# Performance work log

Hardware: AMD Instinct MI355X
Metric: run time of the kernel (lower is better)

The kernel has to match this reference:

```python
import jax, jax.numpy as jnp
import numpy as np

T, B, H, D = 128, 8, 8, 64


def setup_inputs() -> dict:
    key = jax.random.key(0)
    kA, kB, kS = jax.random.split(key, 3)
    # Gated-delta transition matrices: near-identity contractions so the
    # length-T matrix-product recurrence is numerically stable, mimicking
    # A_t = gamma_t * (I - beta_t k_t k_t^T) of the gated delta rule.
    eye = jnp.eye(D, dtype=jnp.float32)
    A = 0.9 * eye + 0.06 * jax.random.normal(kA, (T, B, H, D, D), dtype=jnp.float32)
    Bm = jax.random.normal(kB, (T, B, H, D, D), dtype=jnp.float32)
    init_state = jax.random.normal(kS, (B, H, D, D), dtype=jnp.float32)
    return {"A": A, "Bm": Bm, "init_state": init_state}


def reference(A, Bm, init_state):
    """Gated delta rule recurrence S_t = S_{t-1} @ A_t + B_t for all t,
    computed with a parallel associative scan (Blelloch-equivalent).

    A:  [T,B,H,D,D] transition matrices
    Bm: [T,B,H,D,D] additive updates
    init_state: [B,H,D,D]
    returns states: [T,B,H,D,D]
    """
    def combine(e1, e2):
        # apply e1 first, then e2:
        # (S A1 + B1) A2 + B2 = S (A1 A2) + (B1 A2 + B2)
        A1, B1 = e1
        A2, B2 = e2
        A12 = jnp.einsum('tbhij,tbhjk->tbhik', A1, A2)
        B12 = jnp.einsum('tbhij,tbhjk->tbhik', B1, A2) + B2
        return (A12, B12)

    cumA, cumB = jax.lax.associative_scan(combine, (A, Bm), axis=0)
    # S_t = init_state @ cumA_t + cumB_t
    states = jnp.einsum('bhij,tbhjk->tbhik', init_state, cumA) + cumB
    return states
```

## Files before the change

kernel.cpp:

```cpp
#include <hip/hip_runtime.h>


constexpr int kT = 128;
constexpr int kBH = 64;
constexpr int kD = 64;
constexpr int kTile = kD * kD;
constexpr int kNC = 16;
constexpr int kCH = 8;

typedef __attribute__((ext_vector_type(8))) short short8;
typedef __attribute__((ext_vector_type(4))) float f32x4;
using u32 = unsigned int;

union U8 { u32 u[4]; short8 s; };

__device__ __forceinline__ f32x4 mfma16(short8 a, short8 b, f32x4 c) {
  return __builtin_amdgcn_mfma_f32_16x16x32_bf16(a, b, c, 0, 0, 0);
}

__device__ __forceinline__ void pk_split(float a, float b, u32& h, u32& l) {
  u32 hu;
  asm("v_cvt_pk_bf16_f32 %0, %1, %2" : "=v"(hu) : "v"(a), "v"(b));
  const float ra = a - __uint_as_float(hu << 16);
  const float rb = b - __uint_as_float(hu & 0xffff0000u);
  u32 lu;
  asm("v_cvt_pk_bf16_f32 %0, %1, %2" : "=v"(lu) : "v"(ra), "v"(rb));
  h = hu;
  l = lu;
}

__device__ __forceinline__ short8 gather_frag(u32 p01, u32 p23, u32 q01, u32 q23,
                                              int ad0, int ad1, bool lowh) {
  U8 r;
  int x, y;
  x = __builtin_amdgcn_ds_bpermute(ad0, (int)p01);
  y = __builtin_amdgcn_ds_bpermute(ad0, (int)q01);
  r.u[0] = (u32)(lowh ? x : y);
  x = __builtin_amdgcn_ds_bpermute(ad0, (int)p23);
  y = __builtin_amdgcn_ds_bpermute(ad0, (int)q23);
  r.u[1] = (u32)(lowh ? x : y);
  x = __builtin_amdgcn_ds_bpermute(ad1, (int)p01);
  y = __builtin_amdgcn_ds_bpermute(ad1, (int)q01);
  r.u[2] = (u32)(lowh ? x : y);
  x = __builtin_amdgcn_ds_bpermute(ad1, (int)p23);
  y = __builtin_amdgcn_ds_bpermute(ad1, (int)q23);
  r.u[3] = (u32)(lowh ? x : y);
  return r.s;
}

__device__ __forceinline__ void read_afragT(const float* sAbuf, int row, int k0,
                                            short8& ah, short8& al) {
  const float* base = sAbuf + k0 * 64 + row;
  float d0 = base[0], d1 = base[64], d2 = base[128], d3 = base[192];
  float d4 = base[256], d5 = base[320], d6 = base[384], d7 = base[448];
  U8 h, l;
  u32 hu, lu;
  pk_split(d0, d1, hu, lu); h.u[0] = hu; l.u[0] = lu;
  pk_split(d2, d3, hu, lu); h.u[1] = hu; l.u[1] = lu;
  pk_split(d4, d5, hu, lu); h.u[2] = hu; l.u[2] = lu;
  pk_split(d6, d7, hu, lu); h.u[3] = hu; l.u[3] = lu;
  ah = h.s; al = l.s;
}

#define ISSUE_A(PTRA, SBUF)                                                     \
  do {                                                                          \
    const float* gp_ = (PTRA);                                                  \
    _Pragma("unroll") for (int it_ = 0; it_ < 4; ++it_) {                       \
      const int off_ = (w * 4 + it_) * 256;                                     \
      __builtin_amdgcn_global_load_lds(                                         \
          (const __attribute__((address_space(1))) u32*)(gp_ + off_ + lane * 4),\
          (__attribute__((address_space(3))) u32*)&(SBUF)[off_],                \
          16, 0, 0);                                                            \
    }                                                                           \
  } while (0)

#define LOAD_B4(PTRB)                                                          \
  do {                                                                         \
    const float* Bt_ = (PTRB);                                                 \
    b0 = *reinterpret_cast<const f32x4*>(Bt_ + rowbase + 0 * 16 + q * 4);      \
    b1 = *reinterpret_cast<const f32x4*>(Bt_ + rowbase + 1 * 16 + q * 4);      \
    b2 = *reinterpret_cast<const f32x4*>(Bt_ + rowbase + 2 * 16 + q * 4);      \
    b3 = *reinterpret_cast<const f32x4*>(Bt_ + rowbase + 3 * 16 + q * 4);      \
  } while (0)

#define FOLD_STEP(J, SCUR, SNXT)                                              \
  do {                                                                        \
    const int j_ = (J);                                                       \
    const bool more_ = (j_ + 1 < nS);                                         \
    f32x4 npa[4], npb[4];                                                     \
    npb[0] = b0; npb[1] = b1; npb[2] = b2; npb[3] = b3;                       \
    _Pragma("unroll") for (int cm = 0; cm < 4; ++cm)                          \
        npa[cm] = (f32x4){0.f, 0.f, 0.f, 0.f};                                \
    if (more_) {                                                              \
      ISSUE_A(srcA + (size_t)(e0 + (long)(j_ + 2) * elemStride) * kTile, SNXT); \
      LOAD_B4(srcB + (size_t)(e0 + (long)(j_ + 2) * elemStride) * kTile);     \
      __builtin_amdgcn_sched_barrier(0);                                      \
    }                                                                         \
    _Pragma("unroll") for (int ks = 0; ks < 2; ++ks) {                        \
      u32 pa01h, pa01l, pa23h, pa23l, qa01h, qa01l, qa23h, qa23l;             \
      u32 pb01h, pb01l, pb23h, pb23l, qb01h, qb01l, qb23h, qb23l;             \
      pk_split(apa[2 * ks][0], apa[2 * ks][1], pa01h, pa01l);                 \
      pk_split(apa[2 * ks][2], apa[2 * ks][3], pa23h, pa23l);                 \
      pk_split(apa[2 * ks + 1][0], apa[2 * ks + 1][1], qa01h, qa01l);         \
      pk_split(apa[2 * ks + 1][2], apa[2 * ks + 1][3], qa23h, qa23l);         \
      pk_split(apb[2 * ks][0], apb[2 * ks][1], pb01h, pb01l);                 \
      pk_split(apb[2 * ks][2], apb[2 * ks][3], pb23h, pb23l);                 \
      pk_split(apb[2 * ks + 1][0], apb[2 * ks + 1][1], qb01h, qb01l);         \
      pk_split(apb[2 * ks + 1][2], apb[2 * ks + 1][3], qb23h, qb23l);         \
      const short8 bah = gather_frag(pa01h, pa23h, qa01h, qa23h, ad0, ad1, lowh); \
      const short8 bal = gather_frag(pa01l, pa23l, qa01l, qa23l, ad0, ad1, lowh); \
      const short8 bbh = gather_frag(pb01h, pb23h, qb01h, qb23h, ad0, ad1, lowh); \
      const short8 bbl = gather_frag(pb01l, pb23l, qb01l, qb23l, ad0, ad1, lowh); \
      _Pragma("unroll") for (int cm = 0; cm < 4; ++cm) {                      \
        short8 ah, al;                                                        \
        read_afragT(&(SCUR)[0], cm * 16 + l15, ks * 32 + q * 8, ah, al);      \
        npa[cm] = mfma16(ah, bah, npa[cm]);                                   \
        npa[cm] = mfma16(ah, bal, npa[cm]);                                   \
        npa[cm] = mfma16(al, bah, npa[cm]);                                   \
        npb[cm] = mfma16(ah, bbh, npb[cm]);                                   \
        npb[cm] = mfma16(ah, bbl, npb[cm]);                                   \
        npb[cm] = mfma16(al, bbh, npb[cm]);                                   \
      }                                                                       \
    }                                                                         \
    _Pragma("unroll") for (int cm = 0; cm < 4; ++cm) {                        \
      apa[cm] = npa[cm];                                                      \
      apb[cm] = npb[cm];                                                      \
    }                                                                         \
    if (more_) __syncthreads();                                               \
  } while (0)

__global__ __attribute__((amdgpu_flat_work_group_size(256, 256),
                          amdgpu_waves_per_eu(4, 4)))
void gdr_fold(const float* __restrict__ srcA, const float* __restrict__ srcB,
              float* __restrict__ dstA, float* __restrict__ dstB,
              int perChain, long chainBase, long idxBase, long elemStride,
              int nElem) {
  __shared__ float sA0[4096], sA1[4096];

  const int tid = threadIdx.x;
  const int lane = tid & 63, w = tid >> 6;
  const int q = lane >> 4, l15 = lane & 15;
  const int bh = blockIdx.x / perChain, id = blockIdx.x % perChain;
  const long e0 = (long)bh * chainBase + (long)id * idxBase;
  const int rowbase = (w * 16 + l15) * 64;
  const int ad0 = (l15 + ((lane >> 4) & 1) * 32) * 4;
  const int ad1 = ad0 + 64;
  const bool lowh = lane < 32;
  const int nS = nElem - 1;

  f32x4 apa[4], apb[4];
  {
    const float* At = srcA + (size_t)e0 * kTile;
    const float* Bt = srcB + (size_t)e0 * kTile;
#pragma unroll
    for (int cm = 0; cm < 4; ++cm) {
      apa[cm] = *reinterpret_cast<const f32x4*>(At + rowbase + cm * 16 + q * 4);
      apb[cm] = *reinterpret_cast<const f32x4*>(Bt + rowbase + cm * 16 + q * 4);
    }
  }

  f32x4 b0, b1, b2, b3;
  ISSUE_A(srcA + (size_t)(e0 + elemStride) * kTile, sA0);
  LOAD_B4(srcB + (size_t)(e0 + elemStride) * kTile);
  __syncthreads();

  int j = 0;
  while (true) {
    FOLD_STEP(j, sA0, sA1);
    if (++j >= nS) break;
    FOLD_STEP(j, sA1, sA0);
    if (++j >= nS) break;
  }

  float* pao = dstA + (size_t)blockIdx.x * kTile;
  float* pbo = dstB + (size_t)blockIdx.x * kTile;
#pragma unroll
  for (int cm = 0; cm < 4; ++cm) {
    *reinterpret_cast<f32x4*>(pao + rowbase + cm * 16 + q * 4) = apa[cm];
    *reinterpret_cast<f32x4*>(pbo + rowbase + cm * 16 + q * 4) = apb[cm];
  }
}

#define SCAN_STEP(I, SCUR, SNXT)                                              \
  do {                                                                        \
    const int i_ = (I);                                                       \
    const bool more_ = (i_ + 1 < nSteps);                                     \
    f32x4 nacc[4];                                                            \
    nacc[0] = b0; nacc[1] = b1; nacc[2] = b2; nacc[3] = b3;                   \
    if (more_) {                                                              \
      ISSUE_A(srcA + (size_t)(e0 + (long)(i_ + 1) * elemStride) * kTile, SNXT); \
      LOAD_B4(srcB + (size_t)(e0 + (long)(i_ + 1) * elemStride) * kTile);     \
      __builtin_amdgcn_sched_barrier(0);                                      \
    }                                                                         \
    _Pragma("unroll") for (int ks = 0; ks < 2; ++ks) {                        \
      u32 p01h, p01l, p23h, p23l, q01h, q01l, q23h, q23l;                     \
      pk_split(acc[2 * ks][0], acc[2 * ks][1], p01h, p01l);                   \
      pk_split(acc[2 * ks][2], acc[2 * ks][3], p23h, p23l);                   \
      pk_split(acc[2 * ks + 1][0], acc[2 * ks + 1][1], q01h, q01l);           \
      pk_split(acc[2 * ks + 1][2], acc[2 * ks + 1][3], q23h, q23l);           \
      const short8 bfh = gather_frag(p01h, p23h, q01h, q23h, ad0, ad1, lowh); \
      const short8 bfl = gather_frag(p01l, p23l, q01l, q23l, ad0, ad1, lowh); \
      _Pragma("unroll") for (int cm = 0; cm < 4; ++cm) {                      \
        short8 ah, al;                                                        \
        read_afragT(&(SCUR)[0], cm * 16 + l15, ks * 32 + q * 8, ah, al);      \
        nacc[cm] = mfma16(ah, bfh, nacc[cm]);                                 \
        nacc[cm] = mfma16(ah, bfl, nacc[cm]);                                 \
        nacc[cm] = mfma16(al, bfh, nacc[cm]);                                 \
      }                                                                       \
    }                                                                         \
    const int t_ = tBase + (i_ + 1) * tStep - 1;                              \
    float* o_ = out + ((size_t)t_ * kBH + bh) * kTile;                        \
    _Pragma("unroll") for (int cm = 0; cm < 4; ++cm) {                        \
      *reinterpret_cast<f32x4*>(o_ + rowbase + cm * 16 + q * 4) = nacc[cm];   \
      acc[cm] = nacc[cm];                                                     \
    }                                                                         \
    if (more_) __syncthreads();                                               \
  } while (0)

__global__ __attribute__((amdgpu_flat_work_group_size(256, 256),
                          amdgpu_waves_per_eu(4, 4)))
void gdr_scan(const float* __restrict__ srcA, const float* __restrict__ srcB,
              const float* __restrict__ S0, float* __restrict__ out,
              int perChain, long chainBase, long idxBase, long elemStride,
              int nSteps, int tbMul, int tStep) {
  __shared__ float sA0[4096], sA1[4096];

  const int tid = threadIdx.x;
  const int lane = tid & 63, w = tid >> 6;
  const int q = lane >> 4, l15 = lane & 15;
  const int bh = blockIdx.x / perChain, id = blockIdx.x % perChain;
  const long e0 = (long)bh * chainBase + (long)id * idxBase;
  const int tBase = id * tbMul;
  const int rowbase = (w * 16 + l15) * 64;
  const int ad0 = (l15 + ((lane >> 4) & 1) * 32) * 4;
  const int ad1 = ad0 + 64;
  const bool lowh = lane < 32;

  f32x4 acc[4];
  {
    const float* Sb = (tBase == 0) ? (S0 + (size_t)bh * kTile)
                                   : (out + ((size_t)(tBase - 1) * kBH + bh) * kTile);
#pragma unroll
    for (int cm = 0; cm < 4; ++cm)
      acc[cm] = *reinterpret_cast<const f32x4*>(Sb + rowbase + cm * 16 + q * 4);
  }

  f32x4 b0, b1, b2, b3;
  ISSUE_A(srcA + (size_t)e0 * kTile, sA0);
  LOAD_B4(srcB + (size_t)e0 * kTile);
  __syncthreads();

  int i = 0;
  while (true) {
    SCAN_STEP(i, sA0, sA1);
    if (++i >= nSteps) break;
    SCAN_STEP(i, sA1, sA0);
    if (++i >= nSteps) break;
  }
}

extern "C" void kernel_launch(void* const* d_in, const int* in_sizes, int n_in,
                              void* d_out, int out_size, void* d_ws, size_t ws_size,
                              hipStream_t stream) {
  const float* A  = (const float*)d_in[0];
  const float* Bm = (const float*)d_in[1];
  const float* S0 = (const float*)d_in[2];
  float* out = (float*)d_out;

  float* PA = (float*)d_ws;
  float* PB = PA + (size_t)kBH * kNC * kTile;

  gdr_fold<<<dim3(kBH * kNC), dim3(256), 0, stream>>>(
      A, Bm, PA, PB, kNC, 1L, (long)kCH * kBH, (long)kBH, kCH);
  gdr_scan<<<dim3(kBH), dim3(256), 0, stream>>>(
      PA, PB, S0, out, 1, (long)kNC, 0L, 1L, kNC, 0, kCH);
  gdr_scan<<<dim3(kBH * kNC), dim3(256), 0, stream>>>(
      A, Bm, S0, out, kNC, 1L, (long)kCH * kBH, (long)kBH, kCH - 1, kCH, 1);
}
```

Before: 161.2 us.

## Triple-buffer A tiles in LDS with partial vmcnt waits instead of full syncs

Moves the fold and scan kernels from double- to triple-buffered LDS for the A tiles, prefetching two steps ahead. B tiles are ping-ponged between two register sets. The full __syncthreads after each step becomes an explicit s_waitcnt vmcnt(N) plus s_barrier, so later loads can stay in flight. The aim is to hide global-load latency on the serial recurrence chain. In exchange it uses more LDS and registers (waves_per_eu relaxed to 3), and correctness depends on the hand-counted vmcnt values.

```diff
diff --git a/kernel.cpp b/kernel.cpp
--- a/kernel.cpp
+++ b/kernel.cpp
@@ -65,37 +65,55 @@
 #define ISSUE_A(PTRA, SBUF)                                                     \
   do {                                                                          \
     const float* gp_ = (PTRA);                                                  \
+    float* sb_ = (SBUF);                                                        \
     _Pragma("unroll") for (int it_ = 0; it_ < 4; ++it_) {                       \
       const int off_ = (w * 4 + it_) * 256;                                     \
       __builtin_amdgcn_global_load_lds(                                         \
           (const __attribute__((address_space(1))) u32*)(gp_ + off_ + lane * 4),\
-          (__attribute__((address_space(3))) u32*)&(SBUF)[off_],                \
+          (__attribute__((address_space(3))) u32*)(sb_ + off_),                 \
           16, 0, 0);                                                            \
     }                                                                           \
   } while (0)
 
-#define LOAD_B4(PTRB)                                                          \
+#define LOAD_B4_INTO(R0, R1, R2, R3, PTRB)                                     \
   do {                                                                         \
     const float* Bt_ = (PTRB);                                                 \
-    b0 = *reinterpret_cast<const f32x4*>(Bt_ + rowbase + 0 * 16 + q * 4);      \
-    b1 = *reinterpret_cast<const f32x4*>(Bt_ + rowbase + 1 * 16 + q * 4);      \
-    b2 = *reinterpret_cast<const f32x4*>(Bt_ + rowbase + 2 * 16 + q * 4);      \
-    b3 = *reinterpret_cast<const f32x4*>(Bt_ + rowbase + 3 * 16 + q * 4);      \
-  } while (0)
-
-#define FOLD_STEP(J, SCUR, SNXT)                                              \
+    R0 = *reinterpret_cast<const f32x4*>(Bt_ + rowbase + 0 * 16 + q * 4);      \
+    R1 = *reinterpret_cast<const f32x4*>(Bt_ + rowbase + 1 * 16 + q * 4);      \
+    R2 = *reinterpret_cast<const f32x4*>(Bt_ + rowbase + 2 * 16 + q * 4);      \
+    R3 = *reinterpret_cast<const f32x4*>(Bt_ + rowbase + 3 * 16 + q * 4);      \
+  } while (0)
+
+#define SB0() __builtin_amdgcn_sched_barrier(0)
+
+#define VM_WAIT_BARRIER(NSTR)                                   \
+  do {                                                          \
+    SB0();                                                      \
+    asm volatile("s_waitcnt vmcnt(" NSTR ")" ::: "memory");     \
+    SB0();                                                      \
+    __builtin_amdgcn_s_barrier();                               \
+    SB0();                                                      \
+  } while (0)
+
+#define FOLD_STEP(J, C0, C1, C2, C3, I0, I1, I2, I3)                          \
   do {                                                                        \
     const int j_ = (J);                                                       \
     const bool more_ = (j_ + 1 < nS);                                         \
+    if (more_) {                                                              \
+      const int eB_ = (j_ + 2 <= eMax) ? j_ + 2 : eMax;                       \
+      const int eA_ = (j_ + 3 <= eMax) ? j_ + 3 : eMax;                       \
+      LOAD_B4_INTO(I0, I1, I2, I3,                                            \
+                   srcB + (size_t)(e0 + (long)eB_ * elemStride) * kTile);     \
+      SB0();                                                                  \
+      ISSUE_A(srcA + (size_t)(e0 + (long)eA_ * elemStride) * kTile,           \
+              &sA[cTgt][0]);                                                  \
+      SB0();                                                                  \
+    }                                                                         \
     f32x4 npa[4], npb[4];                                                     \
-    npb[0] = b0; npb[1] = b1; npb[2] = b2; npb[3] = b3;                       \
+    npb[0] = C0; npb[1] = C1; npb[2] = C2; npb[3] = C3;                       \
     _Pragma("unroll") for (int cm = 0; cm < 4; ++cm)                          \
         npa[cm] = (f32x4){0.f, 0.f, 0.f, 0.f};                                \
-    if (more_) {                                                              \
-      ISSUE_A(srcA + (size_t)(e0 + (long)(j_ + 2) * elemStride) * kTile, SNXT); \
-      LOAD_B4(srcB + (size_t)(e0 + (long)(j_ + 2) * elemStride) * kTile);     \
-      __builtin_amdgcn_sched_barrier(0);                                      \
-    }                                                                         \
+    const float* sCur_ = &sA[cCur][0];                                        \
     _Pragma("unroll") for (int ks = 0; ks < 2; ++ks) {                        \
       u32 pa01h, pa01l, pa23h, pa23l, qa01h, qa01l, qa23h, qa23l;             \
       u32 pb01h, pb01l, pb23h, pb23l, qb01h, qb01l, qb23h, qb23l;             \
@@ -113,7 +131,7 @@
       const short8 bbl = gather_frag(pb01l, pb23l, qb01l, qb23l, ad0, ad1, lowh); \
       _Pragma("unroll") for (int cm = 0; cm < 4; ++cm) {                      \
         short8 ah, al;                                                        \
-        read_afragT(&(SCUR)[0], cm * 16 + l15, ks * 32 + q * 8, ah, al);      \
+        read_afragT(sCur_, cm * 16 + l15, ks * 32 + q * 8, ah, al);           \
         npa[cm] = mfma16(ah, bah, npa[cm]);                                   \
         npa[cm] = mfma16(ah, bal, npa[cm]);                                   \
         npa[cm] = mfma16(al, bah, npa[cm]);                                   \
@@ -126,16 +144,18 @@
       apa[cm] = npa[cm];                                                      \
       apb[cm] = npb[cm];                                                      \
     }                                                                         \
-    if (more_) __syncthreads();                                               \
+    if (more_) VM_WAIT_BARRIER("8");                                          \
+    cCur = (cCur == 2) ? 0 : cCur + 1;                                        \
+    cTgt = (cTgt == 2) ? 0 : cTgt + 1;                                        \
   } while (0)
 
 __global__ __attribute__((amdgpu_flat_work_group_size(256, 256),
-                          amdgpu_waves_per_eu(4, 4)))
+                          amdgpu_waves_per_eu(3, 4)))
 void gdr_fold(const float* __restrict__ srcA, const float* __restrict__ srcB,
               float* __restrict__ dstA, float* __restrict__ dstB,
               int perChain, long chainBase, long idxBase, long elemStride,
               int nElem) {
-  __shared__ float sA0[4096], sA1[4096];
+  __shared__ float sA[3][4096];
 
   const int tid = threadIdx.x;
   const int lane = tid & 63, w = tid >> 6;
@@ -147,6 +167,7 @@
   const int ad1 = ad0 + 64;
   const bool lowh = lane < 32;
   const int nS = nElem - 1;
+  const int eMax = nElem - 1;
 
   f32x4 apa[4], apb[4];
   {
@@ -159,16 +180,28 @@
     }
   }
 
-  f32x4 b0, b1, b2, b3;
-  ISSUE_A(srcA + (size_t)(e0 + elemStride) * kTile, sA0);
-  LOAD_B4(srcB + (size_t)(e0 + elemStride) * kTile);
-  __syncthreads();
-
+  f32x4 r0a, r0b, r0c, r0d;
+  f32x4 r1a, r1b, r1c, r1d;
+
+  {
+    const int e2 = (2 <= eMax) ? 2 : eMax;
+    LOAD_B4_INTO(r1a, r1b, r1c, r1d, srcB + (size_t)(e0 + elemStride) * kTile);
+    SB0();
+    ISSUE_A(srcA + (size_t)(e0 + elemStride) * kTile, &sA[1][0]);
+    ISSUE_A(srcA + (size_t)(e0 + (long)e2 * elemStride) * kTile, &sA[2][0]);
+    SB0();
+    asm volatile("s_waitcnt vmcnt(4)" ::: "memory");
+    SB0();
+    __builtin_amdgcn_s_barrier();
+    SB0();
+  }
+
+  int cCur = 1, cTgt = 0;
   int j = 0;
   while (true) {
-    FOLD_STEP(j, sA0, sA1);
+    FOLD_STEP(j, r1a, r1b, r1c, r1d, r0a, r0b, r0c, r0d);
     if (++j >= nS) break;
-    FOLD_STEP(j, sA1, sA0);
+    FOLD_STEP(j, r0a, r0b, r0c, r0d, r1a, r1b, r1c, r1d);
     if (++j >= nS) break;
   }
 
@@ -181,17 +214,23 @@
   }
 }
 
-#define SCAN_STEP(I, SCUR, SNXT)                                              \
+#define SCAN_STEP(I, C0, C1, C2, C3, I0, I1, I2, I3)                          \
   do {                                                                        \
     const int i_ = (I);                                                       \
     const bool more_ = (i_ + 1 < nSteps);                                     \
+    if (more_) {                                                              \
+      const int eB_ = (i_ + 1 <= eMax) ? i_ + 1 : eMax;                       \
+      const int eA_ = (i_ + 2 <= eMax) ? i_ + 2 : eMax;                       \
+      LOAD_B4_INTO(I0, I1, I2, I3,                                            \
+                   srcB + (size_t)(e0 + (long)eB_ * elemStride) * kTile);     \
+      SB0();                                                                  \
+      ISSUE_A(srcA + (size_t)(e0 + (long)eA_ * elemStride) * kTile,           \
+              &sA[cTgt][0]);                                                  \
+      SB0();                                                                  \
+    }                                                                         \
     f32x4 nacc[4];                                                            \
-    nacc[0] = b0; nacc[1] = b1; nacc[2] = b2; nacc[3] = b3;                   \
-    if (more_) {                                                              \
-      ISSUE_A(srcA + (size_t)(e0 + (long)(i_ + 1) * elemStride) * kTile, SNXT); \
-      LOAD_B4(srcB + (size_t)(e0 + (long)(i_ + 1) * elemStride) * kTile);     \
-      __builtin_amdgcn_sched_barrier(0);                                      \
-    }                                                                         \
+    nacc[0] = C0; nacc[1] = C1; nacc[2] = C2; nacc[3] = C3;                   \
+    const float* sCur_ = &sA[cCur][0];                                        \
     _Pragma("unroll") for (int ks = 0; ks < 2; ++ks) {                        \
       u32 p01h, p01l, p23h, p23l, q01h, q01l, q23h, q23l;                     \
       pk_split(acc[2 * ks][0], acc[2 * ks][1], p01h, p01l);                   \
@@ -202,7 +241,7 @@
       const short8 bfl = gather_frag(p01l, p23l, q01l, q23l, ad0, ad1, lowh); \
       _Pragma("unroll") for (int cm = 0; cm < 4; ++cm) {                      \
         short8 ah, al;                                                        \
-        read_afragT(&(SCUR)[0], cm * 16 + l15, ks * 32 + q * 8, ah, al);      \
+        read_afragT(sCur_, cm * 16 + l15, ks * 32 + q * 8, ah, al);           \
         nacc[cm] = mfma16(ah, bfh, nacc[cm]);                                 \
         nacc[cm] = mfma16(ah, bfl, nacc[cm]);                                 \
         nacc[cm] = mfma16(al, bfh, nacc[cm]);                                 \
@@ -214,16 +253,18 @@
       *reinterpret_cast<f32x4*>(o_ + rowbase + cm * 16 + q * 4) = nacc[cm];   \
       acc[cm] = nacc[cm];                                                     \
     }                                                                         \
-    if (more_) __syncthreads();                                               \
+    if (more_) VM_WAIT_BARRIER("12");                                         \
+    cCur = (cCur == 2) ? 0 : cCur + 1;                                        \
+    cTgt = (cTgt == 2) ? 0 : cTgt + 1;                                        \
   } while (0)
 
 __global__ __attribute__((amdgpu_flat_work_group_size(256, 256),
-                          amdgpu_waves_per_eu(4, 4)))
+                          amdgpu_waves_per_eu(3, 4)))
 void gdr_scan(const float* __restrict__ srcA, const float* __restrict__ srcB,
               const float* __restrict__ S0, float* __restrict__ out,
               int perChain, long chainBase, long idxBase, long elemStride,
               int nSteps, int tbMul, int tStep) {
-  __shared__ float sA0[4096], sA1[4096];
+  __shared__ float sA[3][4096];
 
   const int tid = threadIdx.x;
   const int lane = tid & 63, w = tid >> 6;
@@ -235,6 +276,7 @@
   const int ad0 = (l15 + ((lane >> 4) & 1) * 32) * 4;
   const int ad1 = ad0 + 64;
   const bool lowh = lane < 32;
+  const int eMax = nSteps - 1;
 
   f32x4 acc[4];
   {
@@ -245,16 +287,28 @@
       acc[cm] = *reinterpret_cast<const f32x4*>(Sb + rowbase + cm * 16 + q * 4);
   }
 
-  f32x4 b0, b1, b2, b3;
-  ISSUE_A(srcA + (size_t)e0 * kTile, sA0);
-  LOAD_B4(srcB + (size_t)e0 * kTile);
-  __syncthreads();
-
+  f32x4 r0a, r0b, r0c, r0d;
+  f32x4 r1a, r1b, r1c, r1d;
+
+  {
+    const int e1 = (1 <= eMax) ? 1 : eMax;
+    LOAD_B4_INTO(r0a, r0b, r0c, r0d, srcB + (size_t)e0 * kTile);
+    SB0();
+    ISSUE_A(srcA + (size_t)e0 * kTile, &sA[0][0]);
+    ISSUE_A(srcA + (size_t)(e0 + (long)e1 * elemStride) * kTile, &sA[1][0]);
+    SB0();
+    asm volatile("s_waitcnt vmcnt(4)" ::: "memory");
+    SB0();
+    __builtin_amdgcn_s_barrier();
+    SB0();
+  }
+
+  int cCur = 0, cTgt = 2;
   int i = 0;
   while (true) {
-    SCAN_STEP(i, sA0, sA1);
+    SCAN_STEP(i, r0a, r0b, r0c, r0d, r1a, r1b, r1c, r1d);
     if (++i >= nSteps) break;
-    SCAN_STEP(i, sA1, sA0);
+    SCAN_STEP(i, r1a, r1b, r1c, r1d, r0a, r0b, r0c, r0d);
     if (++i >= nSteps) break;
   }
 }
```

Measured after the change: 172.8 us. +7.2%, slower.

## Halve chunk length, prefetch whole chunk to padded LDS, specialize kernels

Applied to the files above, without the earlier changes.

Changes the three-phase chunked scan from 16 chunks of 8 to 32 chunks of 4. The fold and scan kernels now prefetch all three A tiles of a chunk at once into LDS with a 65-float row pitch, meant to avoid bank conflicts on the transposed fragment reads. They then run fully unrolled with a single barrier instead of a double-buffered loop. The middle sequential scan gets longer (32 steps) but the parallel phases get shorter. LDS use rises, and the 4-byte global_load_lds calls add many more load instructions.

```diff
diff --git a/kernel.cpp b/kernel.cpp
--- a/kernel.cpp
+++ b/kernel.cpp
@@ -5,8 +5,9 @@
 constexpr int kBH = 64;
 constexpr int kD = 64;
 constexpr int kTile = kD * kD;
-constexpr int kNC = 16;
-constexpr int kCH = 8;
+constexpr int kNC = 32;
+constexpr int kCH = 4;
+constexpr int kP = 65;
 
 typedef __attribute__((ext_vector_type(8))) short short8;
 typedef __attribute__((ext_vector_type(4))) float f32x4;
@@ -17,6 +18,8 @@
 __device__ __forceinline__ f32x4 mfma16(short8 a, short8 b, f32x4 c) {
   return __builtin_amdgcn_mfma_f32_16x16x32_bf16(a, b, c, 0, 0, 0);
 }
+
+#define SB0() __builtin_amdgcn_sched_barrier(0)
 
 __device__ __forceinline__ void pk_split(float a, float b, u32& h, u32& l) {
   u32 hu;
@@ -48,11 +51,11 @@
   return r.s;
 }
 
-__device__ __forceinline__ void read_afragT(const float* sAbuf, int row, int k0,
-                                            short8& ah, short8& al) {
-  const float* base = sAbuf + k0 * 64 + row;
-  float d0 = base[0], d1 = base[64], d2 = base[128], d3 = base[192];
-  float d4 = base[256], d5 = base[320], d6 = base[384], d7 = base[448];
+__device__ __forceinline__ void read_afragT65(const float* sAbuf, int row, int k0,
+                                              short8& ah, short8& al) {
+  const float* base = sAbuf + k0 * kP + row;
+  float d0 = base[0 * kP], d1 = base[1 * kP], d2 = base[2 * kP], d3 = base[3 * kP];
+  float d4 = base[4 * kP], d5 = base[5 * kP], d6 = base[6 * kP], d7 = base[7 * kP];
   U8 h, l;
   u32 hu, lu;
   pk_split(d0, d1, hu, lu); h.u[0] = hu; l.u[0] = lu;
@@ -62,40 +65,35 @@
   ah = h.s; al = l.s;
 }
 
-#define ISSUE_A(PTRA, SBUF)                                                     \
+#define ISSUE_A65(PTRA, SBUF)                                                   \
   do {                                                                          \
     const float* gp_ = (PTRA);                                                  \
-    _Pragma("unroll") for (int it_ = 0; it_ < 4; ++it_) {                       \
-      const int off_ = (w * 4 + it_) * 256;                                     \
+    float* sb_ = (SBUF);                                                        \
+    _Pragma("unroll") for (int it_ = 0; it_ < 16; ++it_) {                      \
+      const int row_ = w * 16 + it_;                                            \
       __builtin_amdgcn_global_load_lds(                                         \
-          (const __attribute__((address_space(1))) u32*)(gp_ + off_ + lane * 4),\
-          (__attribute__((address_space(3))) u32*)&(SBUF)[off_],                \
-          16, 0, 0);                                                            \
+          (const __attribute__((address_space(1))) u32*)(gp_ + row_ * 64 + lane), \
+          (__attribute__((address_space(3))) u32*)(sb_ + row_ * kP),            \
+          4, 0, 0);                                                             \
     }                                                                           \
   } while (0)
 
-#define LOAD_B4(PTRB)                                                          \
+#define LOAD_B4_INTO(R0, R1, R2, R3, PTRB)                                     \
   do {                                                                         \
     const float* Bt_ = (PTRB);                                                 \
-    b0 = *reinterpret_cast<const f32x4*>(Bt_ + rowbase + 0 * 16 + q * 4);      \
-    b1 = *reinterpret_cast<const f32x4*>(Bt_ + rowbase + 1 * 16 + q * 4);      \
-    b2 = *reinterpret_cast<const f32x4*>(Bt_ + rowbase + 2 * 16 + q * 4);      \
-    b3 = *reinterpret_cast<const f32x4*>(Bt_ + rowbase + 3 * 16 + q * 4);      \
-  } while (0)
-
-#define FOLD_STEP(J, SCUR, SNXT)                                              \
+    R0 = *reinterpret_cast<const f32x4*>(Bt_ + rowbase + 0 * 16 + q * 4);      \
+    R1 = *reinterpret_cast<const f32x4*>(Bt_ + rowbase + 1 * 16 + q * 4);      \
+    R2 = *reinterpret_cast<const f32x4*>(Bt_ + rowbase + 2 * 16 + q * 4);      \
+    R3 = *reinterpret_cast<const f32x4*>(Bt_ + rowbase + 3 * 16 + q * 4);      \
+  } while (0)
+
+#define STEP_FOLD(SA, C0, C1, C2, C3)                                         \
   do {                                                                        \
-    const int j_ = (J);                                                       \
-    const bool more_ = (j_ + 1 < nS);                                         \
     f32x4 npa[4], npb[4];                                                     \
-    npb[0] = b0; npb[1] = b1; npb[2] = b2; npb[3] = b3;                       \
+    npb[0] = C0; npb[1] = C1; npb[2] = C2; npb[3] = C3;                       \
     _Pragma("unroll") for (int cm = 0; cm < 4; ++cm)                          \
         npa[cm] = (f32x4){0.f, 0.f, 0.f, 0.f};                                \
-    if (more_) {                                                              \
-      ISSUE_A(srcA + (size_t)(e0 + (long)(j_ + 2) * elemStride) * kTile, SNXT); \
-      LOAD_B4(srcB + (size_t)(e0 + (long)(j_ + 2) * elemStride) * kTile);     \
-      __builtin_amdgcn_sched_barrier(0);                                      \
-    }                                                                         \
+    const float* sCur_ = &(SA)[0];                                            \
     _Pragma("unroll") for (int ks = 0; ks < 2; ++ks) {                        \
       u32 pa01h, pa01l, pa23h, pa23l, qa01h, qa01l, qa23h, qa23l;             \
       u32 pb01h, pb01l, pb23h, pb23l, qb01h, qb01l, qb23h, qb23l;             \
@@ -113,7 +111,7 @@
       const short8 bbl = gather_frag(pb01l, pb23l, qb01l, qb23l, ad0, ad1, lowh); \
       _Pragma("unroll") for (int cm = 0; cm < 4; ++cm) {                      \
         short8 ah, al;                                                        \
-        read_afragT(&(SCUR)[0], cm * 16 + l15, ks * 32 + q * 8, ah, al);      \
+        read_afragT65(sCur_, cm * 16 + l15, ks * 32 + q * 8, ah, al);         \
         npa[cm] = mfma16(ah, bah, npa[cm]);                                   \
         npa[cm] = mfma16(ah, bal, npa[cm]);                                   \
         npa[cm] = mfma16(al, bah, npa[cm]);                                   \
@@ -126,27 +124,23 @@
       apa[cm] = npa[cm];                                                      \
       apb[cm] = npb[cm];                                                      \
     }                                                                         \
-    if (more_) __syncthreads();                                               \
   } while (0)
 
 __global__ __attribute__((amdgpu_flat_work_group_size(256, 256),
-                          amdgpu_waves_per_eu(4, 4)))
-void gdr_fold(const float* __restrict__ srcA, const float* __restrict__ srcB,
-              float* __restrict__ dstA, float* __restrict__ dstB,
-              int perChain, long chainBase, long idxBase, long elemStride,
-              int nElem) {
-  __shared__ float sA0[4096], sA1[4096];
+                          amdgpu_waves_per_eu(3, 4)))
+void gdr_fold4(const float* __restrict__ srcA, const float* __restrict__ srcB,
+               float* __restrict__ dstA, float* __restrict__ dstB) {
+  __shared__ float sA1[64 * kP], sA2[64 * kP], sA3[64 * kP];
 
   const int tid = threadIdx.x;
   const int lane = tid & 63, w = tid >> 6;
   const int q = lane >> 4, l15 = lane & 15;
-  const int bh = blockIdx.x / perChain, id = blockIdx.x % perChain;
-  const long e0 = (long)bh * chainBase + (long)id * idxBase;
+  const int bh = blockIdx.x / kNC, ck = blockIdx.x % kNC;
+  const long e0 = (long)bh + (long)ck * (kCH * kBH);
   const int rowbase = (w * 16 + l15) * 64;
   const int ad0 = (l15 + ((lane >> 4) & 1) * 32) * 4;
   const int ad1 = ad0 + 64;
   const bool lowh = lane < 32;
-  const int nS = nElem - 1;
 
   f32x4 apa[4], apb[4];
   {
@@ -158,19 +152,26 @@
       apb[cm] = *reinterpret_cast<const f32x4*>(Bt + rowbase + cm * 16 + q * 4);
     }
   }
-
-  f32x4 b0, b1, b2, b3;
-  ISSUE_A(srcA + (size_t)(e0 + elemStride) * kTile, sA0);
-  LOAD_B4(srcB + (size_t)(e0 + elemStride) * kTile);
-  __syncthreads();
-
-  int j = 0;
-  while (true) {
-    FOLD_STEP(j, sA0, sA1);
-    if (++j >= nS) break;
-    FOLD_STEP(j, sA1, sA0);
-    if (++j >= nS) break;
-  }
+  SB0();
+  ISSUE_A65(srcA + (size_t)(e0 + 1 * kBH) * kTile, sA1);
+  ISSUE_A65(srcA + (size_t)(e0 + 2 * kBH) * kTile, sA2);
+  ISSUE_A65(srcA + (size_t)(e0 + 3 * kBH) * kTile, sA3);
+  SB0();
+  f32x4 r1a, r1b, r1c, r1d, r2a, r2b, r2c, r2d, r3a, r3b, r3c, r3d;
+  LOAD_B4_INTO(r1a, r1b, r1c, r1d, srcB + (size_t)(e0 + 1 * kBH) * kTile);
+  SB0();
+  LOAD_B4_INTO(r2a, r2b, r2c, r2d, srcB + (size_t)(e0 + 2 * kBH) * kTile);
+  SB0();
+  LOAD_B4_INTO(r3a, r3b, r3c, r3d, srcB + (size_t)(e0 + 3 * kBH) * kTile);
+  SB0();
+  asm volatile("s_waitcnt vmcnt(12)" ::: "memory");
+  SB0();
+  __builtin_amdgcn_s_barrier();
+  SB0();
+
+  STEP_FOLD(sA1, r1a, r1b, r1c, r1d);
+  STEP_FOLD(sA2, r2a, r2b, r2c, r2d);
+  STEP_FOLD(sA3, r3a, r3b, r3c, r3d);
 
   float* pao = dstA + (size_t)blockIdx.x * kTile;
   float* pbo = dstB + (size_t)blockIdx.x * kTile;
@@ -181,17 +182,11 @@
   }
 }
 
-#define SCAN_STEP(I, SCUR, SNXT)                                              \
+#define STEP_SCAN(SA, C0, C1, C2, C3, TI)                                     \
   do {                                                                        \
-    const int i_ = (I);                                                       \
-    const bool more_ = (i_ + 1 < nSteps);                                     \
     f32x4 nacc[4];                                                            \
-    nacc[0] = b0; nacc[1] = b1; nacc[2] = b2; nacc[3] = b3;                   \
-    if (more_) {                                                              \
-      ISSUE_A(srcA + (size_t)(e0 + (long)(i_ + 1) * elemStride) * kTile, SNXT); \
-      LOAD_B4(srcB + (size_t)(e0 + (long)(i_ + 1) * elemStride) * kTile);     \
-      __builtin_amdgcn_sched_barrier(0);                                      \
-    }                                                                         \
+    nacc[0] = C0; nacc[1] = C1; nacc[2] = C2; nacc[3] = C3;                   \
+    const float* sCur_ = &(SA)[0];                                            \
     _Pragma("unroll") for (int ks = 0; ks < 2; ++ks) {                        \
       u32 p01h, p01l, p23h, p23l, q01h, q01l, q23h, q23l;                     \
       pk_split(acc[2 * ks][0], acc[2 * ks][1], p01h, p01l);                   \
@@ -202,35 +197,32 @@
       const short8 bfl = gather_frag(p01l, p23l, q01l, q23l, ad0, ad1, lowh); \
       _Pragma("unroll") for (int cm = 0; cm < 4; ++cm) {                      \
         short8 ah, al;                                                        \
-        read_afragT(&(SCUR)[0], cm * 16 + l15, ks * 32 + q * 8, ah, al);      \
+        read_afragT65(sCur_, cm * 16 + l15, ks * 32 + q * 8, ah, al);         \
         nacc[cm] = mfma16(ah, bfh, nacc[cm]);                                 \
         nacc[cm] = mfma16(ah, bfl, nacc[cm]);                                 \
         nacc[cm] = mfma16(al, bfh, nacc[cm]);                                 \
       }                                                                       \
     }                                                                         \
-    const int t_ = tBase + (i_ + 1) * tStep - 1;                              \
+    const int t_ = tBase + (TI);                                              \
     float* o_ = out + ((size_t)t_ * kBH + bh) * kTile;                        \
     _Pragma("unroll") for (int cm = 0; cm < 4; ++cm) {                        \
       *reinterpret_cast<f32x4*>(o_ + rowbase + cm * 16 + q * 4) = nacc[cm];   \
       acc[cm] = nacc[cm];                                                     \
     }                                                                         \
-    if (more_) __syncthreads();                                               \
   } while (0)
 
 __global__ __attribute__((amdgpu_flat_work_group_size(256, 256),
-                          amdgpu_waves_per_eu(4, 4)))
-void gdr_scan(const float* __restrict__ srcA, const float* __restrict__ srcB,
-              const float* __restrict__ S0, float* __restrict__ out,
-              int perChain, long chainBase, long idxBase, long elemStride,
-              int nSteps, int tbMul, int tStep) {
-  __shared__ float sA0[4096], sA1[4096];
+                          amdgpu_waves_per_eu(3, 4)))
+void gdr_scan4(const float* __restrict__ srcA, const float* __restrict__ srcB,
+               const float* __restrict__ S0, float* __restrict__ out) {
+  __shared__ float sA1[64 * kP], sA2[64 * kP], sA3[64 * kP];
 
   const int tid = threadIdx.x;
   const int lane = tid & 63, w = tid >> 6;
   const int q = lane >> 4, l15 = lane & 15;
-  const int bh = blockIdx.x / perChain, id = blockIdx.x % perChain;
-  const long e0 = (long)bh * chainBase + (long)id * idxBase;
-  const int tBase = id * tbMul;
+  const int bh = blockIdx.x / kNC, ck = blockIdx.x % kNC;
+  const long e0 = (long)bh + (long)ck * (kCH * kBH);
+  const int tBase = ck * kCH;
   const int rowbase = (w * 16 + l15) * 64;
   const int ad0 = (l15 + ((lane >> 4) & 1) * 32) * 4;
   const int ad1 = ad0 + 64;
@@ -244,18 +236,125 @@
     for (int cm = 0; cm < 4; ++cm)
       acc[cm] = *reinterpret_cast<const f32x4*>(Sb + rowbase + cm * 16 + q * 4);
   }
+  SB0();
+  ISSUE_A65(srcA + (size_t)e0 * kTile, sA1);
+  ISSUE_A65(srcA + (size_t)(e0 + 1 * kBH) * kTile, sA2);
+  ISSUE_A65(srcA + (size_t)(e0 + 2 * kBH) * kTile, sA3);
+  SB0();
+  f32x4 r1a, r1b, r1c, r1d, r2a, r2b, r2c, r2d, r3a, r3b, r3c, r3d;
+  LOAD_B4_INTO(r1a, r1b, r1c, r1d, srcB + (size_t)e0 * kTile);
+  SB0();
+  LOAD_B4_INTO(r2a, r2b, r2c, r2d, srcB + (size_t)(e0 + 1 * kBH) * kTile);
+  SB0();
+  LOAD_B4_INTO(r3a, r3b, r3c, r3d, srcB + (size_t)(e0 + 2 * kBH) * kTile);
+  SB0();
+  asm volatile("s_waitcnt vmcnt(12)" ::: "memory");
+  SB0();
+  __builtin_amdgcn_s_barrier();
+  SB0();
+
+  STEP_SCAN(sA1, r1a, r1b, r1c, r1d, 0);
+  STEP_SCAN(sA2, r2a, r2b, r2c, r2d, 1);
+  STEP_SCAN(sA3, r3a, r3b, r3c, r3d, 2);
+}
+
+__device__ __forceinline__ void read_afragT64(const float* sAbuf, int row, int k0,
+                                              short8& ah, short8& al) {
+  const float* base = sAbuf + k0 * 64 + row;
+  float d0 = base[0], d1 = base[64], d2 = base[128], d3 = base[192];
+  float d4 = base[256], d5 = base[320], d6 = base[384], d7 = base[448];
+  U8 h, l;
+  u32 hu, lu;
+  pk_split(d0, d1, hu, lu); h.u[0] = hu; l.u[0] = lu;
+  pk_split(d2, d3, hu, lu); h.u[1] = hu; l.u[1] = lu;
+  pk_split(d4, d5, hu, lu); h.u[2] = hu; l.u[2] = lu;
+  pk_split(d6, d7, hu, lu); h.u[3] = hu; l.u[3] = lu;
+  ah = h.s; al = l.s;
+}
+
+#define ISSUE_A16(PTRA, SBUF)                                                   \
+  do {                                                                          \
+    const float* gp_ = (PTRA);                                                  \
+    float* sb_ = (SBUF);                                                        \
+    _Pragma("unroll") for (int it_ = 0; it_ < 4; ++it_) {                       \
+      const int off_ = (w * 4 + it_) * 256;                                     \
+      __builtin_amdgcn_global_load_lds(                                         \
+          (const __attribute__((address_space(1))) u32*)(gp_ + off_ + lane * 4),\
+          (__attribute__((address_space(3))) u32*)(sb_ + off_),                 \
+          16, 0, 0);                                                            \
+    }                                                                           \
+  } while (0)
+
+#define SEQ_STEP(I, SCUR, SNXT)                                               \
+  do {                                                                        \
+    const int i_ = (I);                                                       \
+    const bool more_ = (i_ + 1 < kNC);                                        \
+    f32x4 nacc[4];                                                            \
+    nacc[0] = b0; nacc[1] = b1; nacc[2] = b2; nacc[3] = b3;                   \
+    if (more_) {                                                              \
+      ISSUE_A16(srcA + (size_t)(e0 + i_ + 1) * kTile, SNXT);                  \
+      LOAD_B4_INTO(b0, b1, b2, b3, srcB + (size_t)(e0 + i_ + 1) * kTile);     \
+      SB0();                                                                  \
+    }                                                                         \
+    _Pragma("unroll") for (int ks = 0; ks < 2; ++ks) {                        \
+      u32 p01h, p01l, p23h, p23l, q01h, q01l, q23h, q23l;                     \
+      pk_split(acc[2 * ks][0], acc[2 * ks][1], p01h, p01l);                   \
+      pk_split(acc[2 * ks][2], acc[2 * ks][3], p23h, p23l);                   \
+      pk_split(acc[2 * ks + 1][0], acc[2 * ks + 1][1], q01h, q01l);           \
+      pk_split(acc[2 * ks + 1][2], acc[2 * ks + 1][3], q23h, q23l);           \
+      const short8 bfh = gather_frag(p01h, p23h, q01h, q23h, ad0, ad1, lowh); \
+      const short8 bfl = gather_frag(p01l, p23l, q01l, q23l, ad0, ad1, lowh); \
+      _Pragma("unroll") for (int cm = 0; cm < 4; ++cm) {                      \
+        short8 ah, al;                                                        \
+        read_afragT64(&(SCUR)[0], cm * 16 + l15, ks * 32 + q * 8, ah, al);    \
+        nacc[cm] = mfma16(ah, bfh, nacc[cm]);                                 \
+        nacc[cm] = mfma16(ah, bfl, nacc[cm]);                                 \
+        nacc[cm] = mfma16(al, bfh, nacc[cm]);                                 \
+      }                                                                       \
+    }                                                                         \
+    const int t_ = (i_ + 1) * kCH - 1;                                        \
+    float* o_ = out + ((size_t)t_ * kBH + bh) * kTile;                        \
+    _Pragma("unroll") for (int cm = 0; cm < 4; ++cm) {                        \
+      *reinterpret_cast<f32x4*>(o_ + rowbase + cm * 16 + q * 4) = nacc[cm];   \
+      acc[cm] = nacc[cm];                                                     \
+    }                                                                         \
+    if (more_) __syncthreads();                                               \
+  } while (0)
+
+__global__ __launch_bounds__(256, 4) void gdr_scan_seq(
+    const float* __restrict__ srcA, const float* __restrict__ srcB,
+    const float* __restrict__ S0, float* __restrict__ out) {
+  __shared__ float sA0[4096], sA1b[4096];
+
+  const int tid = threadIdx.x;
+  const int lane = tid & 63, w = tid >> 6;
+  const int q = lane >> 4, l15 = lane & 15;
+  const int bh = blockIdx.x;
+  const long e0 = (long)bh * kNC;
+  const int rowbase = (w * 16 + l15) * 64;
+  const int ad0 = (l15 + ((lane >> 4) & 1) * 32) * 4;
+  const int ad1 = ad0 + 64;
+  const bool lowh = lane < 32;
+
+  f32x4 acc[4];
+  {
+    const float* Sb = S0 + (size_t)bh * kTile;
+#pragma unroll
+    for (int cm = 0; cm < 4; ++cm)
+      acc[cm] = *reinterpret_cast<const f32x4*>(Sb + rowbase + cm * 16 + q * 4);
+  }
 
   f32x4 b0, b1, b2, b3;
-  ISSUE_A(srcA + (size_t)e0 * kTile, sA0);
-  LOAD_B4(srcB + (size_t)e0 * kTile);
+  ISSUE_A16(srcA + (size_t)e0 * kTile, sA0);
+  LOAD_B4_INTO(b0, b1, b2, b3, srcB + (size_t)e0 * kTile);
   __syncthreads();
 
   int i = 0;
   while (true) {
-    SCAN_STEP(i, sA0, sA1);
-    if (++i >= nSteps) break;
-    SCAN_STEP(i, sA1, sA0);
-    if (++i >= nSteps) break;
+    SEQ_STEP(i, sA0, sA1b);
+    if (++i >= kNC) break;
+    SEQ_STEP(i, sA1b, sA0);
+    if (++i >= kNC) break;
   }
 }
 
@@ -270,10 +369,7 @@
   float* PA = (float*)d_ws;
   float* PB = PA + (size_t)kBH * kNC * kTile;
 
-  gdr_fold<<<dim3(kBH * kNC), dim3(256), 0, stream>>>(
-      A, Bm, PA, PB, kNC, 1L, (long)kCH * kBH, (long)kBH, kCH);
-  gdr_scan<<<dim3(kBH), dim3(256), 0, stream>>>(
-      PA, PB, S0, out, 1, (long)kNC, 0L, 1L, kNC, 0, kCH);
-  gdr_scan<<<dim3(kBH * kNC), dim3(256), 0, stream>>>(
-      A, Bm, S0, out, kNC, 1L, (long)kCH * kBH, (long)kBH, kCH - 1, kCH, 1);
-}
+  gdr_fold4<<<dim3(kBH * kNC), dim3(256), 0, stream>>>(A, Bm, PA, PB);
+  gdr_scan_seq<<<dim3(kBH), dim3(256), 0, stream>>>(PA, PB, S0, out);
+  gdr_scan4<<<dim3(kBH * kNC), dim3(256), 0, stream>>>(A, Bm, S0, out);
+}
```

Result: slower. 197.7 us (+22.7%).

## Pad LDS A tiles to stride 65 and replace bpermute gathers with permlane swaps

Applied to the files above, without the earlier changes.

Pads the shared-memory copy of each A tile to a row stride of 65 floats so the transposed column reads in read_afragT spread across LDS banks instead of colliding. Because the padded rows are no longer 16-byte aligned, the global-to-LDS async load now issues sixteen 4-byte transfers per wave instead of four 16-byte ones. Separately, the accumulator-to-B-fragment gather switches from ds_bpermute through LDS to v_permlane32/16_swap register shuffles, which keeps those shuffles off the LDS path. The risks are the larger number of small load instructions and the assumption that the permlane shuffle reproduces the old gather layout exactly.

```diff
diff --git a/kernel.cpp b/kernel.cpp
--- a/kernel.cpp
+++ b/kernel.cpp
@@ -7,6 +7,7 @@
 constexpr int kTile = kD * kD;
 constexpr int kNC = 16;
 constexpr int kCH = 8;
+constexpr int kP = 65;
 
 typedef __attribute__((ext_vector_type(8))) short short8;
 typedef __attribute__((ext_vector_type(4))) float f32x4;
@@ -29,30 +30,34 @@
   l = lu;
 }
 
-__device__ __forceinline__ short8 gather_frag(u32 p01, u32 p23, u32 q01, u32 q23,
-                                              int ad0, int ad1, bool lowh) {
+__device__ __forceinline__ void rowpat(u32 v, u32& oa, u32& ob) {
+  u32 d = v, s = v;
+  asm("v_permlane32_swap_b32 %0, %1" : "+v"(d), "+v"(s));
+  asm("v_permlane16_swap_b32 %0, %1" : "+v"(d), "+v"(s));
+  oa = d;
+  ob = s;
+}
+
+__device__ __forceinline__ short8 gather_frag_pl(u32 p01, u32 p23, u32 q01, u32 q23,
+                                                 bool lowh) {
+  u32 x0a, x0b, x1a, x1b, y0a, y0b, y1a, y1b;
+  rowpat(p01, x0a, x0b);
+  rowpat(p23, x1a, x1b);
+  rowpat(q01, y0a, y0b);
+  rowpat(q23, y1a, y1b);
   U8 r;
-  int x, y;
-  x = __builtin_amdgcn_ds_bpermute(ad0, (int)p01);
-  y = __builtin_amdgcn_ds_bpermute(ad0, (int)q01);
-  r.u[0] = (u32)(lowh ? x : y);
-  x = __builtin_amdgcn_ds_bpermute(ad0, (int)p23);
-  y = __builtin_amdgcn_ds_bpermute(ad0, (int)q23);
-  r.u[1] = (u32)(lowh ? x : y);
-  x = __builtin_amdgcn_ds_bpermute(ad1, (int)p01);
-  y = __builtin_amdgcn_ds_bpermute(ad1, (int)q01);
-  r.u[2] = (u32)(lowh ? x : y);
-  x = __builtin_amdgcn_ds_bpermute(ad1, (int)p23);
-  y = __builtin_amdgcn_ds_bpermute(ad1, (int)q23);
-  r.u[3] = (u32)(lowh ? x : y);
+  r.u[0] = lowh ? x0a : y0a;
+  r.u[1] = lowh ? x1a : y1a;
+  r.u[2] = lowh ? x0b : y0b;
+  r.u[3] = lowh ? x1b : y1b;
   return r.s;
 }
 
-__device__ __forceinline__ void read_afragT(const float* sAbuf, int row, int k0,
-                                            short8& ah, short8& al) {
-  const float* base = sAbuf + k0 * 64 + row;
-  float d0 = base[0], d1 = base[64], d2 = base[128], d3 = base[192];
-  float d4 = base[256], d5 = base[320], d6 = base[384], d7 = base[448];
+__device__ __forceinline__ void read_afragT65(const float* sAbuf, int row, int k0,
+                                              short8& ah, short8& al) {
+  const float* base = sAbuf + k0 * kP + row;
+  float d0 = base[0 * kP], d1 = base[1 * kP], d2 = base[2 * kP], d3 = base[3 * kP];
+  float d4 = base[4 * kP], d5 = base[5 * kP], d6 = base[6 * kP], d7 = base[7 * kP];
   U8 h, l;
   u32 hu, lu;
   pk_split(d0, d1, hu, lu); h.u[0] = hu; l.u[0] = lu;
@@ -62,15 +67,16 @@
   ah = h.s; al = l.s;
 }
 
-#define ISSUE_A(PTRA, SBUF)                                                     \
+#define ISSUE_A65(PTRA, SBUF)                                                   \
   do {                                                                          \
     const float* gp_ = (PTRA);                                                  \
-    _Pragma("unroll") for (int it_ = 0; it_ < 4; ++it_) {                       \
-      const int off_ = (w * 4 + it_) * 256;                                     \
+    float* sb_ = (SBUF);                                                        \
+    _Pragma("unroll") for (int it_ = 0; it_ < 16; ++it_) {                      \
+      const int row_ = w * 16 + it_;                                            \
       __builtin_amdgcn_global_load_lds(                                         \
-          (const __attribute__((address_space(1))) u32*)(gp_ + off_ + lane * 4),\
-          (__attribute__((address_space(3))) u32*)&(SBUF)[off_],                \
-          16, 0, 0);                                                            \
+          (const __attribute__((address_space(1))) u32*)(gp_ + row_ * 64 + lane), \
+          (__attribute__((address_space(3))) u32*)(sb_ + row_ * kP),            \
+          4, 0, 0);                                                             \
     }                                                                           \
   } while (0)
 
@@ -92,7 +98,7 @@
     _Pragma("unroll") for (int cm = 0; cm < 4; ++cm)                          \
         npa[cm] = (f32x4){0.f, 0.f, 0.f, 0.f};                                \
     if (more_) {                                                              \
-      ISSUE_A(srcA + (size_t)(e0 + (long)(j_ + 2) * elemStride) * kTile, SNXT); \
+      ISSUE_A65(srcA + (size_t)(e0 + (long)(j_ + 2) * elemStride) * kTile, SNXT); \
       LOAD_B4(srcB + (size_t)(e0 + (long)(j_ + 2) * elemStride) * kTile);     \
       __builtin_amdgcn_sched_barrier(0);                                      \
     }                                                                         \
@@ -107,13 +113,13 @@
       pk_split(apb[2 * ks][2], apb[2 * ks][3], pb23h, pb23l);                 \
       pk_split(apb[2 * ks + 1][0], apb[2 * ks + 1][1], qb01h, qb01l);         \
       pk_split(apb[2 * ks + 1][2], apb[2 * ks + 1][3], qb23h, qb23l);         \
-      const short8 bah = gather_frag(pa01h, pa23h, qa01h, qa23h, ad0, ad1, lowh); \
-      const short8 bal = gather_frag(pa01l, pa23l, qa01l, qa23l, ad0, ad1, lowh); \
-      const short8 bbh = gather_frag(pb01h, pb23h, qb01h, qb23h, ad0, ad1, lowh); \
-      const short8 bbl = gather_frag(pb01l, pb23l, qb01l, qb23l, ad0, ad1, lowh); \
+      const short8 bah = gather_frag_pl(pa01h, pa23h, qa01h, qa23h, lowh);    \
+      const short8 bal = gather_frag_pl(pa01l, pa23l, qa01l, qa23l, lowh);    \
+      const short8 bbh = gather_frag_pl(pb01h, pb23h, qb01h, qb23h, lowh);    \
+      const short8 bbl = gather_frag_pl(pb01l, pb23l, qb01l, qb23l, lowh);    \
       _Pragma("unroll") for (int cm = 0; cm < 4; ++cm) {                      \
         short8 ah, al;                                                        \
-        read_afragT(&(SCUR)[0], cm * 16 + l15, ks * 32 + q * 8, ah, al);      \
+        read_afragT65(&(SCUR)[0], cm * 16 + l15, ks * 32 + q * 8, ah, al);    \
         npa[cm] = mfma16(ah, bah, npa[cm]);                                   \
         npa[cm] = mfma16(ah, bal, npa[cm]);                                   \
         npa[cm] = mfma16(al, bah, npa[cm]);                                   \
@@ -129,13 +135,11 @@
     if (more_) __syncthreads();                                               \
   } while (0)
 
-__global__ __attribute__((amdgpu_flat_work_group_size(256, 256),
-                          amdgpu_waves_per_eu(4, 4)))
-void gdr_fold(const float* __restrict__ srcA, const float* __restrict__ srcB,
-              float* __restrict__ dstA, float* __restrict__ dstB,
-              int perChain, long chainBase, long idxBase, long elemStride,
-              int nElem) {
-  __shared__ float sA0[4096], sA1[4096];
+__global__ __launch_bounds__(256, 4) void gdr_fold(
+    const float* __restrict__ srcA, const float* __restrict__ srcB,
+    float* __restrict__ dstA, float* __restrict__ dstB,
+    int perChain, long chainBase, long idxBase, long elemStride, int nElem) {
+  __shared__ float sA0[64 * kP], sA1[64 * kP];
 
   const int tid = threadIdx.x;
   const int lane = tid & 63, w = tid >> 6;
@@ -143,8 +147,6 @@
   const int bh = blockIdx.x / perChain, id = blockIdx.x % perChain;
   const long e0 = (long)bh * chainBase + (long)id * idxBase;
   const int rowbase = (w * 16 + l15) * 64;
-  const int ad0 = (l15 + ((lane >> 4) & 1) * 32) * 4;
-  const int ad1 = ad0 + 64;
   const bool lowh = lane < 32;
   const int nS = nElem - 1;
 
@@ -160,7 +162,7 @@
   }
 
   f32x4 b0, b1, b2, b3;
-  ISSUE_A(srcA + (size_t)(e0 + elemStride) * kTile, sA0);
+  ISSUE_A65(srcA + (size_t)(e0 + elemStride) * kTile, sA0);
   LOAD_B4(srcB + (size_t)(e0 + elemStride) * kTile);
   __syncthreads();
 
@@ -188,7 +190,7 @@
     f32x4 nacc[4];                                                            \
     nacc[0] = b0; nacc[1] = b1; nacc[2] = b2; nacc[3] = b3;                   \
     if (more_) {                                                              \
-      ISSUE_A(srcA + (size_t)(e0 + (long)(i_ + 1) * elemStride) * kTile, SNXT); \
+      ISSUE_A65(srcA + (size_t)(e0 + (long)(i_ + 1) * elemStride) * kTile, SNXT); \
       LOAD_B4(srcB + (size_t)(e0 + (long)(i_ + 1) * elemStride) * kTile);     \
       __builtin_amdgcn_sched_barrier(0);                                      \
     }                                                                         \
@@ -198,11 +200,11 @@
       pk_split(acc[2 * ks][2], acc[2 * ks][3], p23h, p23l);                   \
       pk_split(acc[2 * ks + 1][0], acc[2 * ks + 1][1], q01h, q01l);           \
       pk_split(acc[2 * ks + 1][2], acc[2 * ks + 1][3], q23h, q23l);           \
-      const short8 bfh = gather_frag(p01h, p23h, q01h, q23h, ad0, ad1, lowh); \
-      const short8 bfl = gather_frag(p01l, p23l, q01l, q23l, ad0, ad1, lowh); \
+      const short8 bfh = gather_frag_pl(p01h, p23h, q01h, q23h, lowh);        \
+      const short8 bfl = gather_frag_pl(p01l, p23l, q01l, q23l, lowh);        \
       _Pragma("unroll") for (int cm = 0; cm < 4; ++cm) {                      \
         short8 ah, al;                                                        \
-        read_afragT(&(SCUR)[0], cm * 16 + l15, ks * 32 + q * 8, ah, al);      \
+        read_afragT65(&(SCUR)[0], cm * 16 + l15, ks * 32 + q * 8, ah, al);    \
         nacc[cm] = mfma16(ah, bfh, nacc[cm]);                                 \
         nacc[cm] = mfma16(ah, bfl, nacc[cm]);                                 \
         nacc[cm] = mfma16(al, bfh, nacc[cm]);                                 \
@@ -217,13 +219,12 @@
     if (more_) __syncthreads();                                               \
   } while (0)
 
-__global__ __attribute__((amdgpu_flat_work_group_size(256, 256),
-                          amdgpu_waves_per_eu(4, 4)))
-void gdr_scan(const float* __restrict__ srcA, const float* __restrict__ srcB,
-              const float* __restrict__ S0, float* __restrict__ out,
-              int perChain, long chainBase, long idxBase, long elemStride,
-              int nSteps, int tbMul, int tStep) {
-  __shared__ float sA0[4096], sA1[4096];
+__global__ __launch_bounds__(256, 4) void gdr_scan(
+    const float* __restrict__ srcA, const float* __restrict__ srcB,
+    const float* __restrict__ S0, float* __restrict__ out,
+    int perChain, long chainBase, long idxBase, long elemStride,
+    int nSteps, int tbMul, int tStep) {
+  __shared__ float sA0[64 * kP], sA1[64 * kP];
 
   const int tid = threadIdx.x;
   const int lane = tid & 63, w = tid >> 6;
@@ -232,8 +233,6 @@
   const long e0 = (long)bh * chainBase + (long)id * idxBase;
   const int tBase = id * tbMul;
   const int rowbase = (w * 16 + l15) * 64;
-  const int ad0 = (l15 + ((lane >> 4) & 1) * 32) * 4;
-  const int ad1 = ad0 + 64;
   const bool lowh = lane < 32;
 
   f32x4 acc[4];
@@ -246,7 +245,7 @@
   }
 
   f32x4 b0, b1, b2, b3;
-  ISSUE_A(srcA + (size_t)e0 * kTile, sA0);
+  ISSUE_A65(srcA + (size_t)e0 * kTile, sA0);
   LOAD_B4(srcB + (size_t)e0 * kTile);
   __syncthreads();
 
```

Result: faster. 153.6 us (-4.7%).
